# Performance work log

Measured on AMD Instinct MI355X. Metric: run time of the kernel, lower is better.

Reference implementation:

```python
import jax, jax.numpy as jnp
import numpy as np

B, N, D, H, L = 16, 1024, 256, 128, 2  # batch, nodes, feat dim, gcn_hidden, n_layers (D == 2*H)


def setup_inputs() -> dict:
    key = jax.random.key(0)
    ks = jax.random.split(key, 16)
    inp = {
        "gcn_input": jax.random.normal(ks[0], (B, N, D), jnp.float32),
        # scale adjacencies by 1/N so aggregated features stay O(1)
        "latent_adj": jax.random.uniform(ks[1], (B, N, N), jnp.float32) / N,
        "dep_adj": jax.random.uniform(ks[2], (B, N, N), jnp.float32) / N,
        # stacked per-layer parameters (leading dim L); layers share shapes since D == 2*H
        "refine_gate": jax.random.normal(ks[3], (L, D, 1), jnp.float32) * 0.02,
        "gate_W_in": jax.random.normal(ks[4], (L, D, 1), jnp.float32) * 0.02,
        "gate_b_in": jnp.zeros((L, 1), jnp.float32),
        "gate_W_out": jax.random.normal(ks[5], (L, D, 1), jnp.float32) * 0.02,
        "gate_b_out": jnp.zeros((L, 1), jnp.float32),
        "fc_in_W": jax.random.normal(ks[6], (L, H, D), jnp.float32) * 0.02,
        "fc_in_b": jnp.zeros((L, H), jnp.float32),
        "fc_out_W": jax.random.normal(ks[7], (L, H, D), jnp.float32) * 0.02,
        "fc_out_b": jnp.zeros((L, H), jnp.float32),
        "ln_g": jnp.ones((L, 2 * H), jnp.float32),
        "ln_b": jnp.zeros((L, 2 * H), jnp.float32),
    }
    return inp


def _gcn_layer(x, latent, dep, rg, Wgi, bgi, Wgo, bgo, Wi, bi, Wo, bo, g, b):
    # refine gate blends dependency and latent adjacency per source node
    gate = jax.nn.sigmoid(x @ rg)  # [B,N,1]
    A_in = gate * dep + (1.0 - gate) * latent  # [B,N,N]
    A_out = gate * jnp.swapaxes(dep, -1, -2) + (1.0 - gate) * jnp.swapaxes(latent, -1, -2)
    Ax_in = A_in @ x   # [B,N,D]
    Ax_out = A_out @ x
    # gcn gates (scalar bias added after the gated product, as in torch)
    Ax_in = Ax_in * jax.nn.sigmoid(Ax_in @ Wgi) + bgi
    Ax_out = Ax_out * jax.nn.sigmoid(Ax_out @ Wgo) + bgo
    # rec_fc(Ax) + rec_fc(x): weight applied to sum, bias counted twice (faithful)
    h_in = (Ax_in + x) @ Wi.T + 2.0 * bi   # [B,N,H]
    h_out = (Ax_out + x) @ Wo.T + 2.0 * bo
    h = jnp.concatenate([h_in, h_out], axis=-1)  # [B,N,2H]
    mu = jnp.mean(h, axis=-1, keepdims=True)
    var = jnp.var(h, axis=-1, keepdims=True)
    h = (h - mu) * jax.lax.rsqrt(var + 1e-5) * g + b
    return jax.nn.gelu(h, approximate=False)


def reference(gcn_input, latent_adj, dep_adj, refine_gate, gate_W_in, gate_b_in,
              gate_W_out, gate_b_out, fc_in_W, fc_in_b, fc_out_W, fc_out_b, ln_g, ln_b):
    x = gcn_input
    for l in range(refine_gate.shape[0]):  # small fixed layer count
        x = _gcn_layer(x, latent_adj, dep_adj, refine_gate[l],
                       gate_W_in[l], gate_b_in[l], gate_W_out[l], gate_b_out[l],
                       fc_in_W[l], fc_in_b[l], fc_out_W[l], fc_out_b[l],
                       ln_g[l], ln_b[l])
    return x
```

## Files before the change

kernel.cpp:

```cpp
#include <hip/hip_runtime.h>
#include <hip/hip_bf16.h>
#include <cstdint>

#define B_ 16
#define N_ 1024
#define D_ 256
#define H_ 128

typedef unsigned short u16;
typedef __attribute__((ext_vector_type(8))) short bf16x8;
typedef __attribute__((ext_vector_type(4))) float f32x4;

__device__ __forceinline__ u16 f2bf(float f) {
    union { float f; uint32_t u; } v; v.f = f;
    return (u16)((v.u + 0x7FFFu + ((v.u >> 16) & 1u)) >> 16);
}

typedef __attribute__((address_space(3))) void lds_void;
typedef const __attribute__((address_space(1))) void g_void;

__device__ __forceinline__ void gl_lds16(const void* g, void* l) {
    __builtin_amdgcn_global_load_lds((g_void*)g, (lds_void*)l, 16, 0, 0);
}

__global__ __launch_bounds__(256) void k_conv_adj(
    const float* __restrict__ dep, const float* __restrict__ lat,
    u16* __restrict__ depb, u16* __restrict__ latb,
    u16* __restrict__ depTb, u16* __restrict__ latTb)
{
    __shared__ float tile[32][33];
    const int bz = blockIdx.z;
    const int b = bz >> 1;
    const float* src = (bz & 1) ? lat : dep;
    u16* dstN = (bz & 1) ? latb : depb;
    u16* dstT = (bz & 1) ? latTb : depTb;
    const int r0 = blockIdx.y * 32, c0 = blockIdx.x * 32;
    const int t = threadIdx.x;
    const int r = t >> 3, cg = (t & 7) * 4;

    const float4 v = *(const float4*)(src + ((size_t)b * N_ + r0 + r) * N_ + c0 + cg);
    ushort4 nv;
    nv.x = f2bf(v.x); nv.y = f2bf(v.y); nv.z = f2bf(v.z); nv.w = f2bf(v.w);
    *(ushort4*)(dstN + ((size_t)b * N_ + r0 + r) * N_ + c0 + cg) = nv;

    tile[r][cg] = v.x; tile[r][cg + 1] = v.y; tile[r][cg + 2] = v.z; tile[r][cg + 3] = v.w;
    __syncthreads();

    const int orow = t >> 3, ii = (t & 7) * 4;
    ushort4 tv;
    tv.x = f2bf(tile[ii][orow]);     tv.y = f2bf(tile[ii + 1][orow]);
    tv.z = f2bf(tile[ii + 2][orow]); tv.w = f2bf(tile[ii + 3][orow]);
    *(ushort4*)(dstT + ((size_t)b * N_ + c0 + orow) * N_ + r0 + ii) = tv;
}

__global__ __launch_bounds__(256) void k_gate_xt(
    const float* __restrict__ x, const float* __restrict__ rg,
    float* __restrict__ gate, u16* __restrict__ xT)
{
    __shared__ u16 lx[D_][36];
    __shared__ float srg[D_];
    const int b = blockIdx.y, n0 = blockIdx.x * 32;
    const int t = threadIdx.x;
    srg[t] = rg[t];
    __syncthreads();

    const int r = t >> 3, cg = t & 7;
    const float* xrow = x + ((size_t)b * N_ + n0 + r) * D_;
    float dot = 0.f;
    #pragma unroll
    for (int u = 0; u < 8; ++u) {
        const int c = cg * 32 + u * 4;
        const float4 v = *(const float4*)(xrow + c);
        lx[c][r] = f2bf(v.x); lx[c + 1][r] = f2bf(v.y);
        lx[c + 2][r] = f2bf(v.z); lx[c + 3][r] = f2bf(v.w);
        dot += v.x * srg[c] + v.y * srg[c + 1] + v.z * srg[c + 2] + v.w * srg[c + 3];
    }
    dot += __shfl_down(dot, 4, 8);
    dot += __shfl_down(dot, 2, 8);
    dot += __shfl_down(dot, 1, 8);
    if (cg == 0) gate[(size_t)b * N_ + n0 + r] = 1.f / (1.f + expf(-dot));
    __syncthreads();

    #pragma unroll
    for (int i = 0; i < 8; ++i) {
        const int unit = i * 256 + t;
        const int d = unit >> 3, nch = (unit & 7) * 4;
        ushort4 wv;
        wv.x = lx[d][nch];     wv.y = lx[d][nch + 1];
        wv.z = lx[d][nch + 2]; wv.w = lx[d][nch + 3];
        *(ushort4*)(xT + ((size_t)b * D_ + d) * N_ + n0 + nch) = wv;
    }
}

__global__ __launch_bounds__(256) void k_gemm_ax(
    const u16* __restrict__ depb, const u16* __restrict__ latb,
    const u16* __restrict__ depTb, const u16* __restrict__ latTb,
    const u16* __restrict__ xT,
    const float* __restrict__ gate,
    const float* __restrict__ Wgi, const float* __restrict__ Wgo,
    const float* __restrict__ bgi, const float* __restrict__ bgo,
    const float* __restrict__ xcur,
    u16* __restrict__ axin, u16* __restrict__ axout)
{
    __shared__ __align__(16) char smem[33280];
    u16* sA1 = (u16*)smem;
    u16* sA2 = sA1 + 1024;
    u16* sB  = sA2 + 1024;
    float* hbuf = (float*)smem;
    __shared__ float sh_g[32];
    __shared__ float sh_s[32];

    const int b = blockIdx.y;
    const int m0 = blockIdx.x * 32;
    const int z = blockIdx.z;
    const u16* A1 = z ? depTb : depb;
    const u16* A2 = z ? latTb : latb;
    const float* Wg = z ? Wgo : Wgi;
    const float bg0 = z ? bgo[0] : bgi[0];
    u16* outp = z ? axout : axin;

    const int t = threadIdx.x;
    const int lane = t & 63;
    const int w = t >> 6;

    if (t < 32) sh_g[t] = gate[(size_t)b * N_ + m0 + t];

    f32x4 acc1[2][4], acc2[2][4];
    const f32x4 fz = {0.f, 0.f, 0.f, 0.f};
    #pragma unroll
    for (int i = 0; i < 2; ++i)
        #pragma unroll
        for (int j = 0; j < 4; ++j) { acc1[i][j] = fz; acc2[i][j] = fz; }

    const u16* gsrc[5];
    u16* ldst[5];
    #pragma unroll
    for (int ci = 0; ci < 5; ++ci) {
        const int c = w * 5 + ci;
        const int el = lane * 8;
        if (c < 4) {
            const int cc = c & 1;
            const int e = cc * 512 + el;
            const int m = e >> 5, k = e & 31;
            const u16* base = (c < 2) ? A1 : A2;
            gsrc[ci] = base + ((size_t)b * N_ + m0 + m) * N_ + k;
            ldst[ci] = ((c < 2) ? sA1 : sA2) + cc * 512;
        } else {
            const int cc = c - 4;
            const int e = cc * 512 + el;
            const int n = e >> 5, k = e & 31;
            gsrc[ci] = xT + ((size_t)b * D_ + n) * N_ + k;
            ldst[ci] = sB + cc * 512;
        }
    }

    const int mrow = lane & 15;
    const int kg = (lane >> 4) * 8;

    for (int ks = 0; ks < N_ / 32; ++ks) {
        #pragma unroll
        for (int ci = 0; ci < 5; ++ci) gl_lds16(gsrc[ci], ldst[ci]);
        __syncthreads();
        bf16x8 a1[2], a2[2], fb[4];
        #pragma unroll
        for (int mt = 0; mt < 2; ++mt) {
            a1[mt] = *(const bf16x8*)(sA1 + (mt * 16 + mrow) * 32 + kg);
            a2[mt] = *(const bf16x8*)(sA2 + (mt * 16 + mrow) * 32 + kg);
        }
        #pragma unroll
        for (int nt = 0; nt < 4; ++nt)
            fb[nt] = *(const bf16x8*)(sB + (w * 64 + nt * 16 + mrow) * 32 + kg);
        #pragma unroll
        for (int mt = 0; mt < 2; ++mt)
            #pragma unroll
            for (int nt = 0; nt < 4; ++nt) {
                acc1[mt][nt] = __builtin_amdgcn_mfma_f32_16x16x32_bf16(a1[mt], fb[nt], acc1[mt][nt], 0, 0, 0);
                acc2[mt][nt] = __builtin_amdgcn_mfma_f32_16x16x32_bf16(a2[mt], fb[nt], acc2[mt][nt], 0, 0, 0);
            }
        __syncthreads();
        #pragma unroll
        for (int ci = 0; ci < 5; ++ci) gsrc[ci] += 32;
    }

    const int hi = lane >> 4;
    #pragma unroll
    for (int mt = 0; mt < 2; ++mt)
        #pragma unroll
        for (int nt = 0; nt < 4; ++nt) {
            const int col = w * 64 + nt * 16 + mrow;
            #pragma unroll
            for (int rr = 0; rr < 4; ++rr) {
                const int row = mt * 16 + hi * 4 + rr;
                const float g = sh_g[row];
                hbuf[row * 260 + col] = g * acc1[mt][nt][rr] + (1.f - g) * acc2[mt][nt][rr];
            }
        }
    __syncthreads();

    {
        const int rr = t >> 3;
        const int c0 = (t & 7) * 32;
        float dot = 0.f;
        #pragma unroll 8
        for (int u = 0; u < 32; ++u) dot += hbuf[rr * 260 + c0 + u] * Wg[c0 + u];
        dot += __shfl_down(dot, 4, 8);
        dot += __shfl_down(dot, 2, 8);
        dot += __shfl_down(dot, 1, 8);
        if ((t & 7) == 0) sh_s[rr] = 1.f / (1.f + expf(-dot));
    }
    __syncthreads();

    #pragma unroll
    for (int i = 0; i < 16; ++i) {
        const int row = (t >> 7) + i * 2;
        const int c = (t & 127) * 2;
        const float s = sh_s[row];
        const size_t gidx = ((size_t)b * N_ + m0 + row) * D_ + c;
        const float2 xv = *(const float2*)(xcur + gidx);
        const float v0 = hbuf[row * 260 + c] * s + bg0 + xv.x;
        const float v1 = hbuf[row * 260 + c + 1] * s + bg0 + xv.y;
        *(ushort2*)(outp + gidx) = make_ushort2(f2bf(v0), f2bf(v1));
    }
}

__global__ __launch_bounds__(256) void k_fc_ln(
    const u16* __restrict__ axin, const u16* __restrict__ axout,
    const u16* __restrict__ Wib, const u16* __restrict__ Wob,
    const float* __restrict__ bi, const float* __restrict__ bo,
    const float* __restrict__ lg, const float* __restrict__ lb,
    float* __restrict__ outp)
{
    __shared__ __align__(16) char smem[33280];
    u16* sAin = (u16*)smem;
    u16* sAout = sAin + 1024;
    u16* sWi = sAout + 1024;
    u16* sWo = sWi + 4096;
    float* hbuf = (float*)smem;
    __shared__ float sh_mu[32], sh_rs[32];

    const int b = blockIdx.y, m0 = blockIdx.x * 32;
    const int t = threadIdx.x, lane = t & 63, w = t >> 6;
    const int half = w >> 1, wn = w & 1;

    f32x4 acc[2][4];
    const f32x4 fz = {0.f, 0.f, 0.f, 0.f};
    #pragma unroll
    for (int i = 0; i < 2; ++i)
        #pragma unroll
        for (int j = 0; j < 4; ++j) acc[i][j] = fz;

    const u16* gsrc[5];
    u16* ldst[5];
    #pragma unroll
    for (int ci = 0; ci < 5; ++ci) {
        const int c = w * 5 + ci;
        const int el = lane * 8;
        if (c < 4) {
            const int cc = c & 1;
            const int e = cc * 512 + el;
            const int m = e >> 5, k = e & 31;
            const u16* base = (c < 2) ? axin : axout;
            gsrc[ci] = base + ((size_t)b * N_ + m0 + m) * D_ + k;
            ldst[ci] = ((c < 2) ? sAin : sAout) + cc * 512;
        } else {
            const int cc = (c - 4) & 7;
            const int e = cc * 512 + el;
            const int n = e >> 5, k = e & 31;
            const u16* base = (c < 12) ? Wib : Wob;
            gsrc[ci] = base + (size_t)n * D_ + k;
            ldst[ci] = ((c < 12) ? sWi : sWo) + cc * 512;
        }
    }

    const u16* sA = half ? sAout : sAin;
    const u16* sW = half ? sWo : sWi;
    const int mrow = lane & 15;
    const int kg = (lane >> 4) * 8;

    for (int ks = 0; ks < D_ / 32; ++ks) {
        #pragma unroll
        for (int ci = 0; ci < 5; ++ci) gl_lds16(gsrc[ci], ldst[ci]);
        __syncthreads();
        bf16x8 a[2], fb[4];
        #pragma unroll
        for (int mt = 0; mt < 2; ++mt)
            a[mt] = *(const bf16x8*)(sA + (mt * 16 + mrow) * 32 + kg);
        #pragma unroll
        for (int nt = 0; nt < 4; ++nt)
            fb[nt] = *(const bf16x8*)(sW + (wn * 64 + nt * 16 + mrow) * 32 + kg);
        #pragma unroll
        for (int mt = 0; mt < 2; ++mt)
            #pragma unroll
            for (int nt = 0; nt < 4; ++nt)
                acc[mt][nt] = __builtin_amdgcn_mfma_f32_16x16x32_bf16(a[mt], fb[nt], acc[mt][nt], 0, 0, 0);
        __syncthreads();
        #pragma unroll
        for (int ci = 0; ci < 5; ++ci) gsrc[ci] += 32;
    }

    const int hi = lane >> 4;
    #pragma unroll
    for (int mt = 0; mt < 2; ++mt)
        #pragma unroll
        for (int nt = 0; nt < 4; ++nt) {
            const int colh = wn * 64 + nt * 16 + mrow;
            const int col = half * 128 + colh;
            const float bias = 2.f * (half ? bo[colh] : bi[colh]);
            #pragma unroll
            for (int rr = 0; rr < 4; ++rr) {
                const int row = mt * 16 + hi * 4 + rr;
                hbuf[row * 260 + col] = acc[mt][nt][rr] + bias;
            }
        }
    __syncthreads();

    {
        const int rr = t >> 3;
        const int c0 = (t & 7) * 32;
        float s = 0.f, ss = 0.f;
        #pragma unroll 8
        for (int u = 0; u < 32; ++u) {
            const float v = hbuf[rr * 260 + c0 + u];
            s += v; ss += v * v;
        }
        s += __shfl_down(s, 4, 8);  ss += __shfl_down(ss, 4, 8);
        s += __shfl_down(s, 2, 8);  ss += __shfl_down(ss, 2, 8);
        s += __shfl_down(s, 1, 8);  ss += __shfl_down(ss, 1, 8);
        if ((t & 7) == 0) {
            const float mu = s * (1.f / 256.f);
            const float var = ss * (1.f / 256.f) - mu * mu;
            sh_mu[rr] = mu;
            sh_rs[rr] = rsqrtf(var + 1e-5f);
        }
    }
    __syncthreads();

    #pragma unroll
    for (int i = 0; i < 16; ++i) {
        const int row = (t >> 7) + i * 2;
        const int c = (t & 127) * 2;
        const float mu = sh_mu[row], rs = sh_rs[row];
        const float2 gg = *(const float2*)(lg + c);
        const float2 bb = *(const float2*)(lb + c);
        const float v0 = (hbuf[row * 260 + c] - mu) * rs * gg.x + bb.x;
        const float v1 = (hbuf[row * 260 + c + 1] - mu) * rs * gg.y + bb.y;
        const float y0 = 0.5f * v0 * (1.f + erff(v0 * 0.70710678118654752f));
        const float y1 = 0.5f * v1 * (1.f + erff(v1 * 0.70710678118654752f));
        const size_t gidx = ((size_t)b * N_ + m0 + row) * D_ + c;
        *(float2*)(outp + gidx) = make_float2(y0, y1);
    }
}

__global__ __launch_bounds__(256) void k_convw(
    const float* __restrict__ wi, const float* __restrict__ wo,
    u16* __restrict__ wib, u16* __restrict__ wob)
{
    const int i = blockIdx.x * 256 + threadIdx.x;
    wib[i] = f2bf(wi[i]);
    wob[i] = f2bf(wo[i]);
}

extern "C" void kernel_launch(void* const* d_in, const int* in_sizes, int n_in,
                              void* d_out, int out_size, void* d_ws, size_t ws_size,
                              hipStream_t stream)
{
    (void)in_sizes; (void)n_in; (void)out_size; (void)ws_size;

    const float* x0  = (const float*)d_in[0];
    const float* lat = (const float*)d_in[1];
    const float* dep = (const float*)d_in[2];
    const float* rg  = (const float*)d_in[3];
    const float* Wgi = (const float*)d_in[4];
    const float* bgi = (const float*)d_in[5];
    const float* Wgo = (const float*)d_in[6];
    const float* bgo = (const float*)d_in[7];
    const float* fiW = (const float*)d_in[8];
    const float* fib = (const float*)d_in[9];
    const float* foW = (const float*)d_in[10];
    const float* fob = (const float*)d_in[11];
    const float* lng = (const float*)d_in[12];
    const float* lnb = (const float*)d_in[13];

    char* ws = (char*)d_ws;
    size_t off = 0;
    auto alloc = [&](size_t bytes) {
        char* p = ws + off;
        off += (bytes + 255) & ~(size_t)255;
        return p;
    };
    u16* depb  = (u16*)alloc(2ull * B_ * N_ * N_);
    u16* latb  = (u16*)alloc(2ull * B_ * N_ * N_);
    u16* depTb = (u16*)alloc(2ull * B_ * N_ * N_);
    u16* latTb = (u16*)alloc(2ull * B_ * N_ * N_);
    u16* xT    = (u16*)alloc(2ull * B_ * D_ * N_);
    u16* axin  = (u16*)alloc(2ull * B_ * N_ * D_);
    u16* axout = (u16*)alloc(2ull * B_ * N_ * D_);
    float* gate = (float*)alloc(4ull * B_ * N_);
    float* xbuf = (float*)alloc(4ull * B_ * N_ * D_);
    u16* Wib = (u16*)alloc(2ull * H_ * D_);
    u16* Wob = (u16*)alloc(2ull * H_ * D_);

    k_conv_adj<<<dim3(32, 32, 32), 256, 0, stream>>>(dep, lat, depb, latb, depTb, latTb);

    const float* xcur = x0;
    for (int l = 0; l < 2; ++l) {
        k_convw<<<128, 256, 0, stream>>>(fiW + (size_t)l * H_ * D_, foW + (size_t)l * H_ * D_, Wib, Wob);
        k_gate_xt<<<dim3(32, B_), 256, 0, stream>>>(xcur, rg + l * D_, gate, xT);
        k_gemm_ax<<<dim3(32, B_, 2), 256, 0, stream>>>(
            depb, latb, depTb, latTb, xT, gate,
            Wgi + l * D_, Wgo + l * D_, bgi + l, bgo + l,
            xcur, axin, axout);
        const bool last = (l == 1);
        k_fc_ln<<<dim3(32, B_), 256, 0, stream>>>(
            axin, axout, Wib, Wob,
            fib + l * H_, fob + l * H_,
            lng + l * 2 * H_, lnb + l * 2 * H_,
            last ? (float*)d_out : xbuf);
        xcur = xbuf;
    }
}
```

Before: 386.0 us.

## Fuse next-layer gate/transpose into fc_ln and enlarge Ax GEMM M tile

The Ax GEMM tile grows from 32 to 64 rows, so each block reuses the loaded xT tile across twice as many adjacency rows, with the epilogue processed in two 32-row chunks. The per-layer gate/transpose kernel is folded into the fc+LayerNorm epilogue, which now writes the next layer's gate, transposed bf16 x and a row-major bf16 copy of x. The weight conversion is also hoisted into a single launch. This cuts launches and fp32 x traffic. In exchange it adds register pressure from doubled accumulators, halves the grid, and the residual x becomes bf16.

```diff
diff --git a/kernel.cpp b/kernel.cpp
--- a/kernel.cpp
+++ b/kernel.cpp
@@ -14,6 +14,9 @@
 __device__ __forceinline__ u16 f2bf(float f) {
     union { float f; uint32_t u; } v; v.f = f;
     return (u16)((v.u + 0x7FFFu + ((v.u >> 16) & 1u)) >> 16);
+}
+__device__ __forceinline__ float bf2f(u16 h) {
+    union { uint32_t u; float f; } v; v.u = ((uint32_t)h) << 16; return v.f;
 }
 
 typedef __attribute__((address_space(3))) void lds_void;
@@ -55,7 +58,7 @@
 
 __global__ __launch_bounds__(256) void k_gate_xt(
     const float* __restrict__ x, const float* __restrict__ rg,
-    float* __restrict__ gate, u16* __restrict__ xT)
+    float* __restrict__ gate, u16* __restrict__ xT, u16* __restrict__ xrow)
 {
     __shared__ u16 lx[D_][36];
     __shared__ float srg[D_];
@@ -65,14 +68,18 @@
     __syncthreads();
 
     const int r = t >> 3, cg = t & 7;
-    const float* xrow = x + ((size_t)b * N_ + n0 + r) * D_;
+    const float* xrp = x + ((size_t)b * N_ + n0 + r) * D_;
+    u16* xwp = xrow + ((size_t)b * N_ + n0 + r) * D_;
     float dot = 0.f;
     #pragma unroll
     for (int u = 0; u < 8; ++u) {
         const int c = cg * 32 + u * 4;
-        const float4 v = *(const float4*)(xrow + c);
-        lx[c][r] = f2bf(v.x); lx[c + 1][r] = f2bf(v.y);
-        lx[c + 2][r] = f2bf(v.z); lx[c + 3][r] = f2bf(v.w);
+        const float4 v = *(const float4*)(xrp + c);
+        ushort4 wv;
+        wv.x = f2bf(v.x); wv.y = f2bf(v.y); wv.z = f2bf(v.z); wv.w = f2bf(v.w);
+        *(ushort4*)(xwp + c) = wv;
+        lx[c][r] = wv.x; lx[c + 1][r] = wv.y;
+        lx[c + 2][r] = wv.z; lx[c + 3][r] = wv.w;
         dot += v.x * srg[c] + v.y * srg[c + 1] + v.z * srg[c + 2] + v.w * srg[c + 3];
     }
     dot += __shfl_down(dot, 4, 8);
@@ -99,19 +106,19 @@
     const float* __restrict__ gate,
     const float* __restrict__ Wgi, const float* __restrict__ Wgo,
     const float* __restrict__ bgi, const float* __restrict__ bgo,
-    const float* __restrict__ xcur,
+    const u16* __restrict__ xrow,
     u16* __restrict__ axin, u16* __restrict__ axout)
 {
     __shared__ __align__(16) char smem[33280];
     u16* sA1 = (u16*)smem;
-    u16* sA2 = sA1 + 1024;
-    u16* sB  = sA2 + 1024;
+    u16* sA2 = sA1 + 2048;
+    u16* sB  = sA2 + 2048;
     float* hbuf = (float*)smem;
-    __shared__ float sh_g[32];
+    __shared__ float sh_g[64];
     __shared__ float sh_s[32];
 
     const int b = blockIdx.y;
-    const int m0 = blockIdx.x * 32;
+    const int m0 = blockIdx.x * 64;
     const int z = blockIdx.z;
     const u16* A1 = z ? depTb : depb;
     const u16* A2 = z ? latTb : latb;
@@ -123,30 +130,30 @@
     const int lane = t & 63;
     const int w = t >> 6;
 
-    if (t < 32) sh_g[t] = gate[(size_t)b * N_ + m0 + t];
-
-    f32x4 acc1[2][4], acc2[2][4];
+    if (t < 64) sh_g[t] = gate[(size_t)b * N_ + m0 + t];
+
+    f32x4 acc1[4][4], acc2[4][4];
     const f32x4 fz = {0.f, 0.f, 0.f, 0.f};
     #pragma unroll
-    for (int i = 0; i < 2; ++i)
+    for (int i = 0; i < 4; ++i)
         #pragma unroll
         for (int j = 0; j < 4; ++j) { acc1[i][j] = fz; acc2[i][j] = fz; }
 
-    const u16* gsrc[5];
-    u16* ldst[5];
-    #pragma unroll
-    for (int ci = 0; ci < 5; ++ci) {
-        const int c = w * 5 + ci;
+    const u16* gsrc[6];
+    u16* ldst[6];
+    #pragma unroll
+    for (int ci = 0; ci < 6; ++ci) {
+        const int c = w * 6 + ci;
         const int el = lane * 8;
-        if (c < 4) {
-            const int cc = c & 1;
+        if (c < 8) {
+            const int cc = c & 3;
             const int e = cc * 512 + el;
             const int m = e >> 5, k = e & 31;
-            const u16* base = (c < 2) ? A1 : A2;
+            const u16* base = (c < 4) ? A1 : A2;
             gsrc[ci] = base + ((size_t)b * N_ + m0 + m) * N_ + k;
-            ldst[ci] = ((c < 2) ? sA1 : sA2) + cc * 512;
+            ldst[ci] = ((c < 4) ? sA1 : sA2) + cc * 512;
         } else {
-            const int cc = c - 4;
+            const int cc = c - 8;
             const int e = cc * 512 + el;
             const int n = e >> 5, k = e & 31;
             gsrc[ci] = xT + ((size_t)b * D_ + n) * N_ + k;
@@ -159,11 +166,11 @@
 
     for (int ks = 0; ks < N_ / 32; ++ks) {
         #pragma unroll
-        for (int ci = 0; ci < 5; ++ci) gl_lds16(gsrc[ci], ldst[ci]);
-        __syncthreads();
-        bf16x8 a1[2], a2[2], fb[4];
-        #pragma unroll
-        for (int mt = 0; mt < 2; ++mt) {
+        for (int ci = 0; ci < 6; ++ci) gl_lds16(gsrc[ci], ldst[ci]);
+        __syncthreads();
+        bf16x8 a1[4], a2[4], fb[4];
+        #pragma unroll
+        for (int mt = 0; mt < 4; ++mt) {
             a1[mt] = *(const bf16x8*)(sA1 + (mt * 16 + mrow) * 32 + kg);
             a2[mt] = *(const bf16x8*)(sA2 + (mt * 16 + mrow) * 32 + kg);
         }
@@ -171,7 +178,7 @@
         for (int nt = 0; nt < 4; ++nt)
             fb[nt] = *(const bf16x8*)(sB + (w * 64 + nt * 16 + mrow) * 32 + kg);
         #pragma unroll
-        for (int mt = 0; mt < 2; ++mt)
+        for (int mt = 0; mt < 4; ++mt)
             #pragma unroll
             for (int nt = 0; nt < 4; ++nt) {
                 acc1[mt][nt] = __builtin_amdgcn_mfma_f32_16x16x32_bf16(a1[mt], fb[nt], acc1[mt][nt], 0, 0, 0);
@@ -179,47 +186,53 @@
             }
         __syncthreads();
         #pragma unroll
-        for (int ci = 0; ci < 5; ++ci) gsrc[ci] += 32;
+        for (int ci = 0; ci < 6; ++ci) gsrc[ci] += 32;
     }
 
     const int hi = lane >> 4;
     #pragma unroll
-    for (int mt = 0; mt < 2; ++mt)
-        #pragma unroll
-        for (int nt = 0; nt < 4; ++nt) {
-            const int col = w * 64 + nt * 16 + mrow;
+    for (int ch = 0; ch < 2; ++ch) {
+        #pragma unroll
+        for (int mt2 = 0; mt2 < 2; ++mt2) {
+            const int mt = ch * 2 + mt2;
             #pragma unroll
-            for (int rr = 0; rr < 4; ++rr) {
-                const int row = mt * 16 + hi * 4 + rr;
-                const float g = sh_g[row];
-                hbuf[row * 260 + col] = g * acc1[mt][nt][rr] + (1.f - g) * acc2[mt][nt][rr];
+            for (int nt = 0; nt < 4; ++nt) {
+                const int col = w * 64 + nt * 16 + mrow;
+                #pragma unroll
+                for (int rr = 0; rr < 4; ++rr) {
+                    const int row = mt2 * 16 + hi * 4 + rr;
+                    const float g = sh_g[ch * 32 + row];
+                    hbuf[row * 260 + col] = g * acc1[mt][nt][rr] + (1.f - g) * acc2[mt][nt][rr];
+                }
             }
         }
-    __syncthreads();
-
-    {
-        const int rr = t >> 3;
-        const int c0 = (t & 7) * 32;
-        float dot = 0.f;
-        #pragma unroll 8
-        for (int u = 0; u < 32; ++u) dot += hbuf[rr * 260 + c0 + u] * Wg[c0 + u];
-        dot += __shfl_down(dot, 4, 8);
-        dot += __shfl_down(dot, 2, 8);
-        dot += __shfl_down(dot, 1, 8);
-        if ((t & 7) == 0) sh_s[rr] = 1.f / (1.f + expf(-dot));
-    }
-    __syncthreads();
-
-    #pragma unroll
-    for (int i = 0; i < 16; ++i) {
-        const int row = (t >> 7) + i * 2;
-        const int c = (t & 127) * 2;
-        const float s = sh_s[row];
-        const size_t gidx = ((size_t)b * N_ + m0 + row) * D_ + c;
-        const float2 xv = *(const float2*)(xcur + gidx);
-        const float v0 = hbuf[row * 260 + c] * s + bg0 + xv.x;
-        const float v1 = hbuf[row * 260 + c + 1] * s + bg0 + xv.y;
-        *(ushort2*)(outp + gidx) = make_ushort2(f2bf(v0), f2bf(v1));
+        __syncthreads();
+
+        {
+            const int rr = t >> 3;
+            const int c0 = (t & 7) * 32;
+            float dot = 0.f;
+            #pragma unroll 8
+            for (int u = 0; u < 32; ++u) dot += hbuf[rr * 260 + c0 + u] * Wg[c0 + u];
+            dot += __shfl_down(dot, 4, 8);
+            dot += __shfl_down(dot, 2, 8);
+            dot += __shfl_down(dot, 1, 8);
+            if ((t & 7) == 0) sh_s[rr] = 1.f / (1.f + expf(-dot));
+        }
+        __syncthreads();
+
+        #pragma unroll
+        for (int i = 0; i < 16; ++i) {
+            const int row = (t >> 7) + i * 2;
+            const int c = (t & 127) * 2;
+            const float s = sh_s[row];
+            const size_t gidx = ((size_t)b * N_ + m0 + ch * 32 + row) * D_ + c;
+            const ushort2 xv = *(const ushort2*)(xrow + gidx);
+            const float v0 = hbuf[row * 260 + c] * s + bg0 + bf2f(xv.x);
+            const float v1 = hbuf[row * 260 + c + 1] * s + bg0 + bf2f(xv.y);
+            *(ushort2*)(outp + gidx) = make_ushort2(f2bf(v0), f2bf(v1));
+        }
+        __syncthreads();
     }
 }
 
@@ -228,7 +241,10 @@
     const u16* __restrict__ Wib, const u16* __restrict__ Wob,
     const float* __restrict__ bi, const float* __restrict__ bo,
     const float* __restrict__ lg, const float* __restrict__ lb,
-    float* __restrict__ outp)
+    const float* __restrict__ rg_next,
+    float* __restrict__ gate_out, u16* __restrict__ xT_out,
+    u16* __restrict__ xrow_out,
+    float* __restrict__ outf)
 {
     __shared__ __align__(16) char smem[33280];
     u16* sAin = (u16*)smem;
@@ -335,19 +351,63 @@
     }
     __syncthreads();
 
-    #pragma unroll
-    for (int i = 0; i < 16; ++i) {
-        const int row = (t >> 7) + i * 2;
-        const int c = (t & 127) * 2;
-        const float mu = sh_mu[row], rs = sh_rs[row];
-        const float2 gg = *(const float2*)(lg + c);
-        const float2 bb = *(const float2*)(lb + c);
-        const float v0 = (hbuf[row * 260 + c] - mu) * rs * gg.x + bb.x;
-        const float v1 = (hbuf[row * 260 + c + 1] - mu) * rs * gg.y + bb.y;
-        const float y0 = 0.5f * v0 * (1.f + erff(v0 * 0.70710678118654752f));
-        const float y1 = 0.5f * v1 * (1.f + erff(v1 * 0.70710678118654752f));
-        const size_t gidx = ((size_t)b * N_ + m0 + row) * D_ + c;
-        *(float2*)(outp + gidx) = make_float2(y0, y1);
+    if (outf) {
+        #pragma unroll
+        for (int i = 0; i < 16; ++i) {
+            const int row = (t >> 7) + i * 2;
+            const int c = (t & 127) * 2;
+            const float mu = sh_mu[row], rs = sh_rs[row];
+            const float2 gg = *(const float2*)(lg + c);
+            const float2 bb = *(const float2*)(lb + c);
+            const float v0 = (hbuf[row * 260 + c] - mu) * rs * gg.x + bb.x;
+            const float v1 = (hbuf[row * 260 + c + 1] - mu) * rs * gg.y + bb.y;
+            const float y0 = 0.5f * v0 * (1.f + erff(v0 * 0.70710678118654752f));
+            const float y1 = 0.5f * v1 * (1.f + erff(v1 * 0.70710678118654752f));
+            const size_t gidx = ((size_t)b * N_ + m0 + row) * D_ + c;
+            *(float2*)(outf + gidx) = make_float2(y0, y1);
+        }
+    } else {
+        #pragma unroll
+        for (int i = 0; i < 16; ++i) {
+            const int row = (t >> 7) + i * 2;
+            const int c = (t & 127) * 2;
+            const float mu = sh_mu[row], rs = sh_rs[row];
+            const float2 gg = *(const float2*)(lg + c);
+            const float2 bb = *(const float2*)(lb + c);
+            const float v0 = (hbuf[row * 260 + c] - mu) * rs * gg.x + bb.x;
+            const float v1 = (hbuf[row * 260 + c + 1] - mu) * rs * gg.y + bb.y;
+            const float y0 = 0.5f * v0 * (1.f + erff(v0 * 0.70710678118654752f));
+            const float y1 = 0.5f * v1 * (1.f + erff(v1 * 0.70710678118654752f));
+            hbuf[row * 260 + c] = y0;
+            hbuf[row * 260 + c + 1] = y1;
+            const size_t gidx = ((size_t)b * N_ + m0 + row) * D_ + c;
+            *(ushort2*)(xrow_out + gidx) = make_ushort2(f2bf(y0), f2bf(y1));
+        }
+        __syncthreads();
+
+        {
+            const int rr = t >> 3;
+            const int c0 = (t & 7) * 32;
+            float dot = 0.f;
+            #pragma unroll 8
+            for (int u = 0; u < 32; ++u) dot += hbuf[rr * 260 + c0 + u] * rg_next[c0 + u];
+            dot += __shfl_down(dot, 4, 8);
+            dot += __shfl_down(dot, 2, 8);
+            dot += __shfl_down(dot, 1, 8);
+            if ((t & 7) == 0) gate_out[(size_t)b * N_ + m0 + rr] = 1.f / (1.f + expf(-dot));
+        }
+
+        #pragma unroll
+        for (int i = 0; i < 8; ++i) {
+            const int unit = i * 256 + t;
+            const int d = unit >> 3, nch = (unit & 7) * 4;
+            ushort4 wv;
+            wv.x = f2bf(hbuf[nch * 260 + d]);
+            wv.y = f2bf(hbuf[(nch + 1) * 260 + d]);
+            wv.z = f2bf(hbuf[(nch + 2) * 260 + d]);
+            wv.w = f2bf(hbuf[(nch + 3) * 260 + d]);
+            *(ushort4*)(xT_out + ((size_t)b * D_ + d) * N_ + m0 + nch) = wv;
+        }
     }
 }
 
@@ -393,29 +453,31 @@
     u16* depTb = (u16*)alloc(2ull * B_ * N_ * N_);
     u16* latTb = (u16*)alloc(2ull * B_ * N_ * N_);
     u16* xT    = (u16*)alloc(2ull * B_ * D_ * N_);
+    u16* xrow  = (u16*)alloc(2ull * B_ * N_ * D_);
     u16* axin  = (u16*)alloc(2ull * B_ * N_ * D_);
     u16* axout = (u16*)alloc(2ull * B_ * N_ * D_);
     float* gate = (float*)alloc(4ull * B_ * N_);
-    float* xbuf = (float*)alloc(4ull * B_ * N_ * D_);
-    u16* Wib = (u16*)alloc(2ull * H_ * D_);
-    u16* Wob = (u16*)alloc(2ull * H_ * D_);
+    u16* Wib = (u16*)alloc(2ull * 2 * H_ * D_);
+    u16* Wob = (u16*)alloc(2ull * 2 * H_ * D_);
 
     k_conv_adj<<<dim3(32, 32, 32), 256, 0, stream>>>(dep, lat, depb, latb, depTb, latTb);
-
-    const float* xcur = x0;
+    k_convw<<<256, 256, 0, stream>>>(fiW, foW, Wib, Wob);
+    k_gate_xt<<<dim3(32, B_), 256, 0, stream>>>(x0, rg, gate, xT, xrow);
+
     for (int l = 0; l < 2; ++l) {
-        k_convw<<<128, 256, 0, stream>>>(fiW + (size_t)l * H_ * D_, foW + (size_t)l * H_ * D_, Wib, Wob);
-        k_gate_xt<<<dim3(32, B_), 256, 0, stream>>>(xcur, rg + l * D_, gate, xT);
-        k_gemm_ax<<<dim3(32, B_, 2), 256, 0, stream>>>(
+        k_gemm_ax<<<dim3(16, B_, 2), 256, 0, stream>>>(
             depb, latb, depTb, latTb, xT, gate,
             Wgi + l * D_, Wgo + l * D_, bgi + l, bgo + l,
-            xcur, axin, axout);
+            xrow, axin, axout);
         const bool last = (l == 1);
         k_fc_ln<<<dim3(32, B_), 256, 0, stream>>>(
-            axin, axout, Wib, Wob,
+            axin, axout, Wib + (size_t)l * H_ * D_, Wob + (size_t)l * H_ * D_,
             fib + l * H_, fob + l * H_,
             lng + l * 2 * H_, lnb + l * 2 * H_,
-            last ? (float*)d_out : xbuf);
-        xcur = xbuf;
-    }
-}
+            rg + (l + 1 < 2 ? (l + 1) * D_ : 0),
+            last ? nullptr : gate,
+            last ? nullptr : xT,
+            last ? nullptr : xrow,
+            last ? (float*)d_out : nullptr);
+    }
+}
```

Result: slower. 408.2 us (+5.7%).
